# Performance work log

Hardware: AMD Instinct MI355X
Metric: run time of the kernel (lower is better)

The kernel has to match this reference:

```python
import jax, jax.numpy as jnp
import numpy as np

TEMPERATURE = 0.07
EPS = 1e-12  # matches torch F.normalize default eps


def setup_inputs() -> dict:
    key = jax.random.key(0)
    k1, k2 = jax.random.split(key)
    features1 = jax.random.normal(k1, (16384, 512), dtype=jnp.float32)
    features2 = jax.random.normal(k2, (16384, 512), dtype=jnp.float32)
    return {"features1": features1, "features2": features2}


def _l2_normalize(x):
    # torch F.normalize: x / max(||x||, eps)
    norm = jnp.sqrt(jnp.sum(x * x, axis=1, keepdims=True))
    return x / jnp.maximum(norm, EPS)


def reference(features1, features2):
    f1 = _l2_normalize(features1)
    f2 = _l2_normalize(features2)
    # [N, N] similarity logits
    logits = jnp.einsum('nd,md->nm', f1, f2) / TEMPERATURE
    n = logits.shape[0]
    # cross-entropy with labels = arange(n): mean over rows of (logsumexp - diag logit)
    log_probs = jax.nn.log_softmax(logits, axis=1)
    diag = jnp.diagonal(log_probs)
    loss = -jnp.mean(diag)
    return loss
```

## Files before the change

kernel.cpp:

```cpp
#include <hip/hip_runtime.h>
#include <stdint.h>

#define NROWS 16384
#define KDIM  512
#define BM 256
#define BN 256
#define CT 2
#define NCHUNK 32
#define NPHASE 16
#define INV_T 14.285714285714286f
#define LOG2E 1.4426950408889634f
#define LN2   0.6931471805599453f

typedef __bf16 bf16x8 __attribute__((ext_vector_type(8)));
typedef float  f32x16 __attribute__((ext_vector_type(16)));
typedef unsigned short u16x8 __attribute__((ext_vector_type(8)));

__device__ __forceinline__ void gload_lds16(const void* gptr, void* lptr) {
    uint32_t loff = (uint32_t)(uintptr_t)lptr;
    loff = __builtin_amdgcn_readfirstlane(loff);
    __builtin_amdgcn_global_load_lds(
        (const uint32_t __attribute__((address_space(1)))*)(uintptr_t)gptr,
        (uint32_t __attribute__((address_space(3)))*)(uintptr_t)loff,
        16, 0, 0);
}


__global__ void k_norm(const float* __restrict__ X, char* __restrict__ Y, float scale) {
    const int row  = blockIdx.x * 4 + (threadIdx.x >> 6);
    const int lane = threadIdx.x & 63;
    const float* xr = X + (size_t)row * KDIM + lane * 8;
    float4 a = *(const float4*)xr;
    float4 b = *(const float4*)(xr + 4);
    float ss = a.x*a.x + a.y*a.y + a.z*a.z + a.w*a.w
             + b.x*b.x + b.y*b.y + b.z*b.z + b.w*b.w;
    #pragma unroll
    for (int off = 1; off < 64; off <<= 1) ss += __shfl_xor(ss, off);
    const float s = scale / fmaxf(sqrtf(ss), 1e-12f);
    __bf16 o[8];
    o[0] = (__bf16)(a.x * s); o[1] = (__bf16)(a.y * s);
    o[2] = (__bf16)(a.z * s); o[3] = (__bf16)(a.w * s);
    o[4] = (__bf16)(b.x * s); o[5] = (__bf16)(b.y * s);
    o[6] = (__bf16)(b.z * s); o[7] = (__bf16)(b.w * s);
    const int kh = lane >> 2, q = lane & 3;
    const size_t gr = ((size_t)(kh * 512 + (row >> 5)) * 2 + (q >> 1)) * 64
                    + ((q & 1) << 5) + (row & 31);
    *(u16x8*)(Y + gr * 16) = *(const u16x8*)o;
}

__global__ __launch_bounds__(512, 1) void k_gemm(const char* __restrict__ A,
                                                 const char* __restrict__ B,
                                                 float* __restrict__ S_part) {
    __shared__ __align__(16) char L[4 * 32768];
    __shared__ float rowsum[4][BM];

    const int tid  = threadIdx.x;
    const int lane = tid & 63;
    const int w    = tid >> 6;
    const int wr   = w >> 2, wc = w & 3;
    const int bid  = blockIdx.x;
    const int xcd  = bid & 7;
    const int idx  = bid >> 3;
    const int st   = idx >> 5;
    const int wsub = idx & 31;
    const int brow  = (st * 8 + (wsub >> 2)) * BM;
    const int chunk = xcd * 4 + (wsub & 3);

    const int lbyte = lane * 16;

#define STAGE(h_, s_) do {                                               \
        const char* ga_ = A + (size_t)((h_) * NROWS + brow) * 64 + tid * 16; \
        const char* gb_ = B + (size_t)((h_) * NROWS + bcol) * 64 + tid * 16; \
        char* la_ = L + (s_) * 32768 + tid * 16;                         \
        gload_lds16(ga_,        la_);                                    \
        gload_lds16(ga_ + 8192, la_ + 8192);                             \
        gload_lds16(gb_,        la_ + 16384);                            \
        gload_lds16(gb_ + 8192, la_ + 24576);                            \
    } while (0)

    float rowacc = 0.f;
    for (int ct = 0; ct < CT; ++ct) {
        const int bcol = (chunk * CT + ct) * BN;
        f32x16 acc[4][2] = {};

        STAGE(0, 0);
        STAGE(1, 1);
        asm volatile("s_waitcnt vmcnt(4)" ::: "memory");
        __builtin_amdgcn_s_barrier();

        #pragma unroll
        for (int h = 0; h < NPHASE; ++h) {
            const char* sl = L + (h & 3) * 32768;
            bf16x8 af[4][2], bf[2][2];
            #pragma unroll
            for (int m = 0; m < 4; ++m)
                #pragma unroll
                for (int ks = 0; ks < 2; ++ks)
                    af[m][ks] = *(const bf16x8*)(sl + ((wr * 4 + m) * 2 + ks) * 1024 + lbyte);
            #pragma unroll
            for (int n = 0; n < 2; ++n)
                #pragma unroll
                for (int ks = 0; ks < 2; ++ks)
                    bf[n][ks] = *(const bf16x8*)(sl + 16384 + ((wc * 2 + n) * 2 + ks) * 1024 + lbyte);
            if (h < NPHASE - 2) STAGE(h + 2, (h + 2) & 3);
            __builtin_amdgcn_sched_barrier(0);
            if (h < NPHASE - 2)       asm volatile("s_waitcnt vmcnt(4)" ::: "memory");
            else if (h == NPHASE - 2) asm volatile("s_waitcnt vmcnt(0)" ::: "memory");
            __builtin_amdgcn_s_barrier();
            asm volatile("s_waitcnt lgkmcnt(0)" ::: "memory");
            __builtin_amdgcn_sched_barrier(0);
            __builtin_amdgcn_s_setprio(1);
            #pragma unroll
            for (int m = 0; m < 4; ++m)
                #pragma unroll
                for (int n = 0; n < 2; ++n)
                    #pragma unroll
                    for (int ks = 0; ks < 2; ++ks)
                        acc[m][n] = __builtin_amdgcn_mfma_f32_32x32x16_bf16(
                            af[m][ks], bf[n][ks], acc[m][n], 0, 0, 0);
            __builtin_amdgcn_s_setprio(0);
            __builtin_amdgcn_s_barrier();
        }

        #pragma unroll
        for (int m = 0; m < 4; ++m) {
            float rs[16];
            #pragma unroll
            for (int r = 0; r < 16; ++r)
                rs[r] = __builtin_amdgcn_exp2f(acc[m][0][r])
                      + __builtin_amdgcn_exp2f(acc[m][1][r]);
            #pragma unroll
            for (int off = 16; off >= 1; off >>= 1)
                #pragma unroll
                for (int r = 0; r < 16; ++r)
                    rs[r] += __shfl_xor(rs[r], off);
            if ((lane & 31) == 0) {
                const int rb = wr * 128 + m * 32 + (lane >> 5) * 4;
                #pragma unroll
                for (int r = 0; r < 16; ++r)
                    rowsum[wc][rb + (r & 3) + 8 * (r >> 2)] = rs[r];
            }
        }
        __syncthreads();
        if (tid < BM)
            rowacc += rowsum[0][tid] + rowsum[1][tid] + rowsum[2][tid] + rowsum[3][tid];
        __syncthreads();
    }
#undef STAGE
    if (tid < BM) S_part[(size_t)chunk * NROWS + brow + tid] = rowacc;
}

__global__ void k_diag(const char* __restrict__ A, const char* __restrict__ B,
                       float* __restrict__ diag) {
    const int row  = blockIdx.x * 4 + (threadIdx.x >> 6);
    const int lane = threadIdx.x & 63;
    const int kh = lane >> 2, q = lane & 3;
    const size_t gr = ((size_t)(kh * 512 + (row >> 5)) * 2 + (q >> 1)) * 64
                    + ((q & 1) << 5) + (row & 31);
    const bf16x8 va = *(const bf16x8*)(A + gr * 16);
    const bf16x8 vb = *(const bf16x8*)(B + gr * 16);
    float d = 0.f;
    #pragma unroll
    for (int i = 0; i < 8; ++i) d += (float)va[i] * (float)vb[i];
    #pragma unroll
    for (int off2 = 1; off2 < 64; off2 <<= 1) d += __shfl_xor(d, off2);
    if (lane == 0) diag[row] = d;
}

__global__ void k_loss(const float* __restrict__ S_part, const float* __restrict__ diag,
                       float* __restrict__ partial) {
    const int g = blockIdx.x * 256 + threadIdx.x;
    float S = 0.f;
    #pragma unroll
    for (int c = 0; c < NCHUNK; ++c) S += S_part[(size_t)c * NROWS + g];
    float v = logf(S) - diag[g] * LN2;
    __shared__ float wsum[4];
    #pragma unroll
    for (int off = 1; off < 64; off <<= 1) v += __shfl_xor(v, off);
    if ((threadIdx.x & 63) == 0) wsum[threadIdx.x >> 6] = v;
    __syncthreads();
    if (threadIdx.x == 0) partial[blockIdx.x] = wsum[0] + wsum[1] + wsum[2] + wsum[3];
}

__global__ void k_final(const float* __restrict__ partial, float* __restrict__ out) {
    float v = partial[threadIdx.x];
    #pragma unroll
    for (int off = 1; off < 64; off <<= 1) v += __shfl_xor(v, off);
    if (threadIdx.x == 0) out[0] = v * (1.0f / (float)NROWS);
}

extern "C" void kernel_launch(void* const* d_in, const int* in_sizes, int n_in,
                              void* d_out, int out_size, void* d_ws, size_t ws_size,
                              hipStream_t stream) {
    const float* f1 = (const float*)d_in[0];
    const float* f2 = (const float*)d_in[1];
    float* out = (float*)d_out;

    char* ws = (char*)d_ws;
    char*  f1p   = ws;
    char*  f2p   = ws + (16u << 20);
    float* S_part = (float*)(ws + (32u << 20));
    float* diag   = (float*)(ws + (34u << 20));
    float* part   = (float*)(ws + (34u << 20) + (1u << 16));

    k_norm<<<dim3(NROWS / 4), dim3(256), 0, stream>>>(f1, f1p, INV_T * LOG2E);
    k_norm<<<dim3(NROWS / 4), dim3(256), 0, stream>>>(f2, f2p, 1.0f);
    k_gemm<<<dim3((NROWS / BM) * NCHUNK), dim3(512), 0, stream>>>(f1p, f2p, S_part);
    k_diag<<<dim3(NROWS / 4), dim3(256), 0, stream>>>(f1p, f2p, diag);
    k_loss<<<dim3(NROWS / 256), dim3(256), 0, stream>>>(S_part, diag, part);
    k_final<<<dim3(1), dim3(64), 0, stream>>>(part, out);
}
```

Before: 398.6 us.

## Shrink GEMM column tile to 128 and run two blocks per CU

Halves the B tile width (BN 256→128, four column tiles per block), remaps the eight waves to a 4x2 grid so each wave holds a 64x64 accumulator, and trims the LDS stage to 24 KB so two workgroups can be resident per CU. The block-to-tile swizzle is also reworked to group row and chunk assignment by XCD. The aim is better latency hiding through occupancy and lower register pressure. The cost is lower arithmetic intensity per LDS load, since A is reloaded for every column tile, plus more epilogue passes.

```diff
diff --git a/kernel.cpp b/kernel.cpp
--- a/kernel.cpp
+++ b/kernel.cpp
@@ -4,10 +4,10 @@
 #define NROWS 16384
 #define KDIM  512
 #define BM 256
-#define BN 256
-#define CT 2
+#define BN 128
+#define CT 4
 #define NCHUNK 32
-#define NPHASE 16
+#define NPH 16
 #define INV_T 14.285714285714286f
 #define LOG2E 1.4426950408889634f
 #define LN2   0.6931471805599453f
@@ -48,70 +48,78 @@
     *(u16x8*)(Y + gr * 16) = *(const u16x8*)o;
 }
 
-__global__ __launch_bounds__(512, 1) void k_gemm(const char* __restrict__ A,
+__global__ __launch_bounds__(512, 2) void k_gemm(const char* __restrict__ A,
                                                  const char* __restrict__ B,
                                                  float* __restrict__ S_part) {
-    __shared__ __align__(16) char L[4 * 32768];
-    __shared__ float rowsum[4][BM];
+    __shared__ __align__(16) char L[4 * 24576];
+    __shared__ float rowsum[2][BM];
+    char* Lc = (char*)L;
 
     const int tid  = threadIdx.x;
     const int lane = tid & 63;
     const int w    = tid >> 6;
-    const int wr   = w >> 2, wc = w & 3;
+    const int wr   = w >> 1, wc = w & 1;
     const int bid  = blockIdx.x;
     const int xcd  = bid & 7;
     const int idx  = bid >> 3;
     const int st   = idx >> 5;
     const int wsub = idx & 31;
-    const int brow  = (st * 8 + (wsub >> 2)) * BM;
-    const int chunk = xcd * 4 + (wsub & 3);
-
-    const int lbyte = lane * 16;
-
-#define STAGE(h_, s_) do {                                               \
-        const char* ga_ = A + (size_t)((h_) * NROWS + brow) * 64 + tid * 16; \
-        const char* gb_ = B + (size_t)((h_) * NROWS + bcol) * 64 + tid * 16; \
-        char* la_ = L + (s_) * 32768 + tid * 16;                         \
-        gload_lds16(ga_,        la_);                                    \
-        gload_lds16(ga_ + 8192, la_ + 8192);                             \
-        gload_lds16(gb_,        la_ + 16384);                            \
-        gload_lds16(gb_ + 8192, la_ + 24576);                            \
+    const int sg   = xcd * 8 + st;
+    const int bg   = sg & 7, cg = sg >> 3;
+    const int brow  = (bg * 8 + (wsub >> 2)) * BM;
+    const int chunk = cg * 4 + (wsub & 3);
+    const int rbA0 = brow >> 5;
+
+#define STGA(KH_, S_) do {                                                    \
+        const char* g_ = A + ((size_t)((KH_) * 512 + rbA0) * 2048) + tid * 16;\
+        char* l_ = Lc + (S_) * 24576 + tid * 16;                              \
+        gload_lds16(g_,        l_);                                           \
+        gload_lds16(g_ + 8192, l_ + 8192);                                    \
     } while (0)
 
+#define STGB(KH_, S_) do {                                                    \
+        const char* g_ = B + ((size_t)((KH_) * 512 + rbB0) * 2048) + tid * 16;\
+        char* l_ = Lc + (S_) * 24576 + 16384 + tid * 16;                      \
+        gload_lds16(g_, l_);                                                  \
+    } while (0)
+
     float rowacc = 0.f;
+    #pragma unroll 1
     for (int ct = 0; ct < CT; ++ct) {
-        const int bcol = (chunk * CT + ct) * BN;
-        f32x16 acc[4][2] = {};
-
-        STAGE(0, 0);
-        STAGE(1, 1);
-        asm volatile("s_waitcnt vmcnt(4)" ::: "memory");
+        const int rbB0 = (chunk * 16 + ct * 4);
+        f32x16 acc[2][2] = {};
+        bf16x8 af[2][2], bf[2][2];
+
+        STGA(0, 0); STGB(0, 0);
+        STGA(1, 1); STGB(1, 1);
+        asm volatile("s_waitcnt vmcnt(3)" ::: "memory");
         __builtin_amdgcn_s_barrier();
 
         #pragma unroll
-        for (int h = 0; h < NPHASE; ++h) {
-            const char* sl = L + (h & 3) * 32768;
-            bf16x8 af[4][2], bf[2][2];
-            #pragma unroll
-            for (int m = 0; m < 4; ++m)
+        for (int h = 0; h < NPH; ++h) {
+            const char* sl = Lc + (h & 3) * 24576;
+            #pragma unroll
+            for (int m = 0; m < 2; ++m)
                 #pragma unroll
                 for (int ks = 0; ks < 2; ++ks)
-                    af[m][ks] = *(const bf16x8*)(sl + ((wr * 4 + m) * 2 + ks) * 1024 + lbyte);
+                    af[m][ks] = *(const bf16x8*)(sl + ((wr * 2 + m) << 11)
+                                                 + (ks << 10) + (lane << 4));
             #pragma unroll
             for (int n = 0; n < 2; ++n)
                 #pragma unroll
                 for (int ks = 0; ks < 2; ++ks)
-                    bf[n][ks] = *(const bf16x8*)(sl + 16384 + ((wc * 2 + n) * 2 + ks) * 1024 + lbyte);
-            if (h < NPHASE - 2) STAGE(h + 2, (h + 2) & 3);
+                    bf[n][ks] = *(const bf16x8*)(sl + 16384 + ((wc * 2 + n) << 11)
+                                                 + (ks << 10) + (lane << 4));
+            if (h < NPH - 2) { STGA(h + 2, (h + 2) & 3); STGB(h + 2, (h + 2) & 3); }
             __builtin_amdgcn_sched_barrier(0);
-            if (h < NPHASE - 2)       asm volatile("s_waitcnt vmcnt(4)" ::: "memory");
-            else if (h == NPHASE - 2) asm volatile("s_waitcnt vmcnt(0)" ::: "memory");
+            if (h < NPH - 2)       asm volatile("s_waitcnt vmcnt(3)" ::: "memory");
+            else if (h == NPH - 2) asm volatile("s_waitcnt vmcnt(0)" ::: "memory");
             __builtin_amdgcn_s_barrier();
             asm volatile("s_waitcnt lgkmcnt(0)" ::: "memory");
             __builtin_amdgcn_sched_barrier(0);
             __builtin_amdgcn_s_setprio(1);
             #pragma unroll
-            for (int m = 0; m < 4; ++m)
+            for (int m = 0; m < 2; ++m)
                 #pragma unroll
                 for (int n = 0; n < 2; ++n)
                     #pragma unroll
@@ -123,7 +131,7 @@
         }
 
         #pragma unroll
-        for (int m = 0; m < 4; ++m) {
+        for (int m = 0; m < 2; ++m) {
             float rs[16];
             #pragma unroll
             for (int r = 0; r < 16; ++r)
@@ -135,18 +143,18 @@
                 for (int r = 0; r < 16; ++r)
                     rs[r] += __shfl_xor(rs[r], off);
             if ((lane & 31) == 0) {
-                const int rb = wr * 128 + m * 32 + (lane >> 5) * 4;
+                const int rb = wr * 64 + m * 32 + (lane >> 5) * 4;
                 #pragma unroll
                 for (int r = 0; r < 16; ++r)
                     rowsum[wc][rb + (r & 3) + 8 * (r >> 2)] = rs[r];
             }
         }
         __syncthreads();
-        if (tid < BM)
-            rowacc += rowsum[0][tid] + rowsum[1][tid] + rowsum[2][tid] + rowsum[3][tid];
+        if (tid < BM) rowacc += rowsum[0][tid] + rowsum[1][tid];
         __syncthreads();
     }
-#undef STAGE
+#undef STGA
+#undef STGB
     if (tid < BM) S_part[(size_t)chunk * NROWS + brow + tid] = rowacc;
 }
 
```

Measured after the change: 370.5 us. 7.1% less time.
